# Kernel optimization log

Measured on AMD Instinct MI355X. Metric: run time of the kernel, lower is better.

## Reference

```python
import jax, jax.numpy as jnp
import numpy as np
from math import factorial, comb

N_NODES = 50000
N_EDGES = 640000
FEAT = 32
NUM_BASIS = 8
CUTOFF = 5.0
MAX_Z = 118
NUM_ITERS = 3
LMAX = 2
K = (LMAX + 1) ** 2  # 9 spherical channels for max_degree=2


def _assoc_legendre(c, s, lmax):
    # associated Legendre P_l^m without Condon-Shortley phase
    P = {(0, 0): np.ones_like(c)}
    for m in range(1, lmax + 1):
        P[(m, m)] = P[(m - 1, m - 1)] * (2 * m - 1) * s
    for m in range(lmax):
        P[(m + 1, m)] = (2 * m + 1) * c * P[(m, m)]
    for m in range(lmax + 1):
        for l in range(m + 2, lmax + 1):
            P[(l, m)] = ((2 * l - 1) * c * P[(l - 1, m)] - (l + m - 1) * P[(l - 2, m)]) / (l - m)
    return P


def _real_sh_np(xyz, lmax):
    # Racah-normalized real spherical harmonics (Y_00 = 1), order m=-l..l
    r = np.linalg.norm(xyz, axis=1)
    cth = xyz[:, 2] / r
    sth = np.sqrt(np.maximum(1.0 - cth ** 2, 0.0))
    phi = np.arctan2(xyz[:, 1], xyz[:, 0])
    P = _assoc_legendre(cth, sth, lmax)
    cols = []
    for l in range(lmax + 1):
        for m in range(-l, l + 1):
            am = abs(m)
            if m == 0:
                cols.append(P[(l, 0)])
            else:
                nrm = np.sqrt(2.0 * factorial(l - am) / factorial(l + am))
                ang = np.cos(am * phi) if m > 0 else np.sin(am * phi)
                cols.append(nrm * P[(l, am)] * ang)
    return np.stack(cols, axis=1)


def _gaunt_tensor():
    # cg[k1,k2,k3]: expansion of Y_k1 * Y_k2 onto Y_k3 (degrees <= 2).
    # Products of degree<=2 harmonics lie exactly in span of degree<=4 harmonics,
    # so the least-squares fit below recovers exact coefficients.
    rng = np.random.default_rng(0)
    pts = rng.normal(size=(4096, 3))
    pts /= np.linalg.norm(pts, axis=1, keepdims=True)
    A = _real_sh_np(pts, 2 * LMAX)  # (M, 25)
    Y = A[:, :K]                    # (M, 9)
    prod = (Y[:, :, None] * Y[:, None, :]).reshape(len(pts), K * K)
    coef, *_ = np.linalg.lstsq(A, prod, rcond=None)  # (25, 81)
    return coef[:K].reshape(K, K, K).transpose(1, 2, 0).astype(np.float32)


CG = jnp.asarray(_gaunt_tensor())  # (9, 9, 9)
LOG_BINOM = jnp.asarray([np.log(comb(NUM_BASIS - 1, kk)) for kk in range(NUM_BASIS)], dtype=jnp.float32)


def _sh_l2(u):
    # Racah real SH of unit vectors, degrees 0..2, order m=-l..l
    x, y, z = u[:, 0], u[:, 1], u[:, 2]
    s3 = 1.7320508075688772
    return jnp.stack([
        jnp.ones_like(x),
        y, z, x,
        s3 * x * y, s3 * y * z, 0.5 * (3.0 * z * z - 1.0), s3 * x * z, 0.5 * s3 * (x * x - y * y),
    ], axis=1)


def _radial(r):
    # reciprocal Bernstein basis (log-space, stable) * smooth cutoff
    u = r / (1.0 + r)
    k = jnp.arange(NUM_BASIS, dtype=jnp.float32)
    n = float(NUM_BASIS - 1)
    eps = 1e-12
    logu = jnp.log(jnp.maximum(u, eps))[:, None]
    log1u = jnp.log(jnp.maximum(1.0 - u, eps))[:, None]
    bern = jnp.exp(LOG_BINOM + k * logu + (n - k) * log1u)  # (E, B)
    cut = jnp.where(r < CUTOFF, jnp.exp(-(r * r) / jnp.maximum(CUTOFF * CUTOFF - r * r, eps)), 0.0)
    return bern * cut[:, None]


def _forward(dr_vec, embed, rad_w, d1w, d1b, d2w, d2b, Z, neighbor_idxs):
    idx_i, idx_j = neighbor_idxs[0], neighbor_idxs[1]
    r = jnp.linalg.norm(dr_vec, axis=1)
    u = dr_vec / jnp.maximum(r, 1e-9)[:, None]
    Ysh = _sh_l2(u)              # (E, 9) angular basis
    rad = _radial(r)             # (E, B) radial basis
    # mask padding edges (idx_i == idx_j) as in mask_by_neighbor
    rad = rad * (idx_i != idx_j).astype(rad.dtype)[:, None]

    N = Z.shape[0]
    x = jnp.zeros((N, K, FEAT), jnp.float32).at[:, 0, :].set(embed[Z])

    for i in range(NUM_ITERS):
        last = i == NUM_ITERS - 1
        k3 = 1 if last else K    # last MessagePass has max_degree=0
        xe = x[idx_j]                                  # (E, 9, F) edge gather
        g = jnp.einsum('eb,dbf->edf', rad, rad_w[i])   # (E, 3, F) radial->feature per basis degree
        y = jnp.zeros((N_EDGES, k3, FEAT), jnp.float32)
        for l2 in range(LMAX + 1):
            sl = slice(l2 * l2, (l2 + 1) ** 2)
            c = jnp.einsum('abc,eb->eac', CG[:, sl, :k3], Ysh[:, sl])          # (E, 9, k3)
            y = y + jnp.einsum('eac,eaf->ecf', c, xe * g[:, l2][:, None, :])   # (E, k3, F)
        m = jax.ops.segment_sum(y, idx_i, num_segments=N)                      # scatter-sum
        if last:
            x = x[:, :1, :]      # change_max_degree_or_type(x, 0)
        h = x + m
        h = jnp.einsum('nkf,fg->nkg', h, d1w[i]).at[:, 0, :].add(d1b[i])
        gate = jax.nn.sigmoid(h[:, :1, :])
        h = h * gate             # silu on scalar channel, sigmoid-gated tensor channels
        h = jnp.einsum('nkf,fg->nkg', h, d2w[i]).at[:, 0, :].add(d2b[i])
        x = x + h
    return x[:, 0, :]            # (N, F)


def setup_inputs() -> dict:
    key = jax.random.key(0)
    ks = jax.random.split(key, 8)
    dr_vec = jax.random.normal(ks[0], (N_EDGES, 3), jnp.float32) * 2.0
    Z = jax.random.randint(ks[1], (N_NODES,), 0, MAX_Z + 1, jnp.int32)
    neighbor_idxs = jax.random.randint(ks[2], (2, N_EDGES), 0, N_NODES, jnp.int32)
    embed = jax.random.normal(ks[3], (MAX_Z + 1, FEAT), jnp.float32)
    rad_w = jax.random.normal(ks[4], (NUM_ITERS, LMAX + 1, NUM_BASIS, FEAT), jnp.float32) * 0.5
    d1w = jax.random.normal(ks[5], (NUM_ITERS, FEAT, FEAT), jnp.float32) * (1.0 / np.sqrt(FEAT))
    d1b = jnp.zeros((NUM_ITERS, FEAT), jnp.float32)
    d2w = jax.random.normal(ks[6], (NUM_ITERS, FEAT, FEAT), jnp.float32) * 0.02
    d2b = jnp.zeros((NUM_ITERS, FEAT), jnp.float32)
    return {"dr_vec": dr_vec, "embed": embed, "rad_w": rad_w, "d1w": d1w, "d1b": d1b,
            "d2w": d2w, "d2b": d2b, "Z": Z, "neighbor_idxs": neighbor_idxs}


def reference(dr_vec, embed, rad_w, d1w, d1b, d2w, d2b, Z, neighbor_idxs):
    return _forward(dr_vec, embed, rad_w, d1w, d1b, d2w, d2b, Z, neighbor_idxs)
```

## Files before the change

kernel.cpp:

```cpp
#include <hip/hip_runtime.h>
#include <hip/hip_fp16.h>
#include <math.h>

#define NN 50000
#define NE 640000
#define F  32
#define KCH 9
#define CUT 5.0f

#define C13 (1.0f/3.0f)
#define C23 (2.0f/3.0f)
#define C15 0.2f
#define C25 0.4f
#define C17 (1.0f/7.0f)
#define C27 (2.0f/7.0f)
#define IS3 0.5773502691896258f
#define S35 0.3464101615137755f
#define S37 0.2474358296526968f
#define S3  1.7320508075688772f

#define XH_NODE_B 768

union U2H { unsigned int u; __half2 h; };

__device__ __forceinline__ unsigned int pack2(float a, float b) {
    U2H c; c.h = __floats2half2_rn(a, b); return c.u;
}
__device__ __forceinline__ float2 unpack2(unsigned int u) {
    U2H c; c.u = u; return __half22float2(c.h);
}

__global__ __launch_bounds__(256) void init_x(const float* __restrict__ embed,
                                              const int* __restrict__ Z,
                                              float* __restrict__ x,
                                              char* __restrict__ xh) {
    int idx = blockIdx.x * 256 + threadIdx.x;
    int n = idx >> 5, f = idx & 31;
    float v = embed[Z[n] * F + f];
    float* xp = x + (size_t)n * KCH * F + f;
    xp[0] = v;
    #pragma unroll
    for (int a = 1; a < KCH; ++a) xp[a * F] = 0.f;
    char* bp = xh + (size_t)n * XH_NODE_B + f * 24;
    uint2 u0; u0.x = pack2(v, 0.f); u0.y = 0u;
    uint2 zz; zz.x = 0u; zz.y = 0u;
    *(uint2*)bp = u0;
    *(uint2*)(bp + 8) = zz;
    *(uint2*)(bp + 16) = zz;
}

__global__ __launch_bounds__(256) void hist_kernel(const int* __restrict__ idx_i,
                                                   const int* __restrict__ idx_j,
                                                   const float* __restrict__ dr,
                                                   int* __restrict__ cnt) {
    int e = blockIdx.x * 256 + threadIdx.x;
    if (e >= NE) return;
    int ni = idx_i[e], nj = idx_j[e];
    float dx = dr[3 * e + 0], dy = dr[3 * e + 1], dz = dr[3 * e + 2];
    float r2 = fmaf(dx, dx, fmaf(dy, dy, dz * dz));
    if (ni != nj && r2 < CUT * CUT) atomicAdd(&cnt[ni], 1);
}

#define SCAN_T 1024
#define SCAN_C ((NN + SCAN_T - 1) / SCAN_T)

__global__ __launch_bounds__(SCAN_T) void scan_kernel(const int* __restrict__ cnt,
                                                      int* __restrict__ offs,
                                                      int* __restrict__ head) {
    __shared__ int ps[SCAN_T];
    int t = threadIdx.x;
    int b = t * SCAN_C;
    int e = min(b + SCAN_C, NN);
    int s = 0;
    for (int i = b; i < e; ++i) s += cnt[i];
    ps[t] = s;
    __syncthreads();
    for (int off = 1; off < SCAN_T; off <<= 1) {
        int v = (t >= off) ? ps[t - off] : 0;
        __syncthreads();
        ps[t] += v;
        __syncthreads();
    }
    int run = (t == 0) ? 0 : ps[t - 1];
    for (int i = b; i < e; ++i) { int c = cnt[i]; offs[i] = run; head[i] = run; run += c; }
    if (t == SCAN_T - 1) offs[NN] = ps[SCAN_T - 1];
}

__global__ __launch_bounds__(256) void fill_kernel(const int* __restrict__ idx_i,
                                                   const int* __restrict__ idx_j,
                                                   const float* __restrict__ dr,
                                                   int* __restrict__ head,
                                                   uint2* __restrict__ erec,
                                                   int* __restrict__ njarr) {
    int e = blockIdx.x * 256 + threadIdx.x;
    if (e >= NE) return;
    int ni = idx_i[e], nj = idx_j[e];
    float dx = dr[3 * e + 0], dy = dr[3 * e + 1], dz = dr[3 * e + 2];
    float r2 = fmaf(dx, dx, fmaf(dy, dy, dz * dz));
    if (!(ni != nj && r2 < CUT * CUT)) return;

    float r = sqrtf(r2);
    float inv = 1.0f / fmaxf(r, 1e-9f);
    float ux = dx * inv, uy = dy * inv, uz = dz * inv;

    float cut = expf(-r2 / fmaxf(CUT * CUT - r2, 1e-12f));
    float ur = r / (1.0f + r), vr = 1.0f - ur;
    float up2 = ur*ur, up3 = up2*ur, up4 = up3*ur, up5 = up4*ur, up6 = up5*ur, up7 = up6*ur;
    float vp2 = vr*vr, vp3 = vp2*vr, vp4 = vp3*vr, vp5 = vp4*vr, vp6 = vp5*vr, vp7 = vp6*vr;

    float rc0 = cut * vp7;
    float rc1 = cut * 7.f  * ur  * vp6;
    float rc2 = cut * 21.f * up2 * vp5;
    float rc3 = cut * 35.f * up3 * vp4;
    float rc4 = cut * 35.f * up4 * vp3;
    float rc5 = cut * 21.f * up5 * vp2;
    float rc6 = cut * 7.f  * up6 * vr;
    float rc7 = cut * up7;

    int p = atomicAdd(&head[ni], 1);
    uint2 e0, e1, e2;
    e0.x = pack2(ux, uy); e0.y = pack2(uz, 0.f);
    e1.x = pack2(rc0, rc1); e1.y = pack2(rc2, rc3);
    e2.x = pack2(rc4, rc5); e2.y = pack2(rc6, rc7);
    erec[(size_t)3 * p + 0] = e0;
    erec[(size_t)3 * p + 1] = e1;
    erec[(size_t)3 * p + 2] = e2;
    njarr[p] = nj;
}

template<int LAST>
__global__ __launch_bounds__(256) void gather_kernel(const uint2* __restrict__ erec,
                                                     const int* __restrict__ njarr,
                                                     const char* __restrict__ xh,
                                                     const float* __restrict__ rw_iter,
                                                     const int* __restrict__ offs,
                                                     float* __restrict__ m) {
    const int NWAVES = 2048 * 4;
    int lane = threadIdx.x & 63;
    int wid  = threadIdx.x >> 6;
    int half = lane >> 5;
    int f    = lane & 31;
    int gw   = blockIdx.x * 4 + wid;

    float rwv[24];
    #pragma unroll
    for (int lb = 0; lb < 24; ++lb) rwv[lb] = rw_iter[lb * F + f];
    if (LAST) {
        #pragma unroll
        for (int lb = 8; lb < 16; ++lb) rwv[lb] *= C13;
        #pragma unroll
        for (int lb = 16; lb < 24; ++lb) rwv[lb] *= C15;
    }

    constexpr int NACC = LAST ? 1 : KCH;

    for (int n = gw; n < NN; n += NWAVES) {
        int start = offs[n], end = offs[n + 1];

        float acc[NACC];
        #pragma unroll
        for (int a = 0; a < NACC; ++a) acc[a] = 0.f;

        int t = start + half;
        uint2 xa_c = {}, xb_c = {};
        unsigned int xc_c = 0;
        int nj_n = 0;

        if (t < end) {
            int nj0 = njarr[t];
            const char* bp = xh + (size_t)nj0 * XH_NODE_B + f * 24;
            xa_c = *(const uint2*)bp;
            xb_c = *(const uint2*)(bp + 8);
            xc_c = *(const unsigned int*)(bp + 16);
            int t2 = (t + 2 < end) ? t + 2 : t;
            nj_n = njarr[t2];
        }

        while (t < end) {
            int tn = t + 2;
            int tnc = (tn < end) ? tn : t;
            int tfc = (tn + 2 < end) ? tn + 2 : tnc;

            const char* bp = xh + (size_t)nj_n * XH_NODE_B + f * 24;
            uint2 xa_n = *(const uint2*)bp;
            uint2 xb_n = *(const uint2*)(bp + 8);
            unsigned int xc_n = *(const unsigned int*)(bp + 16);
            int nj_f = njarr[tfc];

            uint2 e0 = erec[(size_t)3 * t + 0];
            uint2 e1 = erec[(size_t)3 * t + 1];
            uint2 e2 = erec[(size_t)3 * t + 2];

            float2 uxy = unpack2(e0.x);
            float ux = uxy.x, uy = uxy.y;
            float uz = unpack2(e0.y).x;
            float2 rcA = unpack2(e1.x);
            float2 rcB = unpack2(e1.y);
            float2 rcC = unpack2(e2.x);
            float2 rcD = unpack2(e2.y);

            float xe[9];
            {
                float2 p;
                p = unpack2(xa_c.x); xe[0] = p.x; xe[1] = p.y;
                p = unpack2(xa_c.y); xe[2] = p.x; xe[3] = p.y;
                p = unpack2(xb_c.x); xe[4] = p.x; xe[5] = p.y;
                p = unpack2(xb_c.y); xe[6] = p.x; xe[7] = p.y;
                p = unpack2(xc_c);   xe[8] = p.x;
            }

            float g0, g1, g2;
            g0 = rcA.x * rwv[0];
            g0 = fmaf(rcA.y, rwv[1], g0); g0 = fmaf(rcB.x, rwv[2], g0); g0 = fmaf(rcB.y, rwv[3], g0);
            g0 = fmaf(rcC.x, rwv[4], g0); g0 = fmaf(rcC.y, rwv[5], g0); g0 = fmaf(rcD.x, rwv[6], g0);
            g0 = fmaf(rcD.y, rwv[7], g0);
            g1 = rcA.x * rwv[8];
            g1 = fmaf(rcA.y, rwv[9],  g1); g1 = fmaf(rcB.x, rwv[10], g1); g1 = fmaf(rcB.y, rwv[11], g1);
            g1 = fmaf(rcC.x, rwv[12], g1); g1 = fmaf(rcC.y, rwv[13], g1); g1 = fmaf(rcD.x, rwv[14], g1);
            g1 = fmaf(rcD.y, rwv[15], g1);
            g2 = rcA.x * rwv[16];
            g2 = fmaf(rcA.y, rwv[17], g2); g2 = fmaf(rcB.x, rwv[18], g2); g2 = fmaf(rcB.y, rwv[19], g2);
            g2 = fmaf(rcC.x, rwv[20], g2); g2 = fmaf(rcC.y, rwv[21], g2); g2 = fmaf(rcD.x, rwv[22], g2);
            g2 = fmaf(rcD.y, rwv[23], g2);

            if (LAST) {
                float dot1 = uy * xe[1];
                dot1 = fmaf(uz, xe[2], dot1);
                dot1 = fmaf(ux, xe[3], dot1);
                float Y4 = S3 * ux * uy, Y5 = S3 * uy * uz, Y7 = S3 * ux * uz;
                float Y6 = fmaf(1.5f * uz, uz, -0.5f);
                float Y8 = 0.5f * S3 * (ux * ux - uy * uy);
                float dot2 = Y4 * xe[4];
                dot2 = fmaf(Y5, xe[5], dot2);
                dot2 = fmaf(Y6, xe[6], dot2);
                dot2 = fmaf(Y7, xe[7], dot2);
                dot2 = fmaf(Y8, xe[8], dot2);
                acc[0] = fmaf(g0, xe[0], acc[0]);
                acc[0] = fmaf(g1, dot1, acc[0]);
                acc[0] = fmaf(g2, dot2, acc[0]);
            } else {
                float s2 = S3 * g2;
                float w[9];
                w[0] = g0;
                w[1] = uy * g1; w[2] = uz * g1; w[3] = ux * g1;
                w[4] = s2 * ux * uy;
                w[5] = s2 * uy * uz;
                w[6] = fmaf(1.5f * uz, uz, -0.5f) * g2;
                w[7] = s2 * ux * uz;
                w[8] = 0.5f * s2 * (ux * ux - uy * uy);

                float d0 = xe[0]*w[0], d1 = xe[1]*w[1], d2 = xe[2]*w[2], d3 = xe[3]*w[3];
                float d4 = xe[4]*w[4], d5 = xe[5]*w[5], d6 = xe[6]*w[6], d7 = xe[7]*w[7];
                float d8 = xe[8]*w[8];

                acc[0] += d0 + C13 * (d1 + d2 + d3) + C15 * (d4 + d5 + d6 + d7 + d8);
                #define T(a, b) (xe[a] * w[b] + xe[b] * w[a])
                acc[1] += T(0,1) - C15 * T(1,6) - S35 * T(1,8) + S35 * T(2,5) + S35 * T(3,4);
                acc[2] += T(0,2) + S35 * T(1,5) + C25 * T(2,6) + S35 * T(3,7);
                acc[3] += T(0,3) + S35 * T(1,4) + S35 * T(2,7) - C15 * T(3,6) + S35 * T(3,8);
                acc[4] += T(0,4) + IS3 * T(1,3) - C27 * T(4,6) + S37 * T(5,7);
                acc[5] += T(0,5) + IS3 * T(1,2) + S37 * T(4,7) + C17 * T(5,6) - S37 * T(5,8);
                acc[6] += T(0,6) - C13 * d1 + C23 * d2 - C13 * d3
                        - C27 * d4 + C17 * d5 + C27 * d6 + C17 * d7 - C27 * d8;
                acc[7] += T(0,7) + IS3 * T(2,3) + S37 * T(4,5) + C17 * T(6,7) + S37 * T(7,8);
                acc[8] += T(0,8) - IS3 * d1 + IS3 * d3 - S37 * d5 + S37 * d7 - C27 * T(6,8);
                #undef T
            }

            xa_c = xa_n; xb_c = xb_n; xc_c = xc_n;
            nj_n = nj_f;
            t = tn;
        }

        #pragma unroll
        for (int a = 0; a < NACC; ++a) acc[a] += __shfl_xor(acc[a], 32);

        if (half == 0) {
            if (LAST) {
                m[(size_t)n * F + f] = acc[0];
            } else {
                float* mp = m + (size_t)n * KCH * F + f;
                #pragma unroll
                for (int a = 0; a < KCH; ++a) mp[a * F] = acc[a];
            }
        }
    }
}

__global__ __launch_bounds__(256) void node_full(float* __restrict__ x,
                                                 const float* __restrict__ m,
                                                 char* __restrict__ xh,
                                                 const float* __restrict__ w1,
                                                 const float* __restrict__ b1,
                                                 const float* __restrict__ w2,
                                                 const float* __restrict__ b2) {
    __shared__ float tile[8][KCH][F];
    int nl = threadIdx.x >> 5, f = threadIdx.x & 31;
    int n = blockIdx.x * 8 + nl;

    float w1c[F];
    #pragma unroll
    for (int fi = 0; fi < F; ++fi) w1c[fi] = w1[fi * F + f];

    float xk[KCH];
    #pragma unroll
    for (int k = 0; k < KCH; ++k) {
        xk[k] = x[((size_t)n * KCH + k) * F + f];
        tile[nl][k][f] = xk[k] + m[((size_t)n * KCH + k) * F + f];
    }
    __syncthreads();

    float o1[KCH];
    #pragma unroll
    for (int k = 0; k < KCH; ++k) {
        float s = 0.f;
        #pragma unroll
        for (int fi = 0; fi < F; ++fi) s = fmaf(tile[nl][k][fi], w1c[fi], s);
        o1[k] = s;
    }
    o1[0] += b1[f];
    float gate = 1.0f / (1.0f + expf(-o1[0]));
    __syncthreads();
    #pragma unroll
    for (int k = 0; k < KCH; ++k) tile[nl][k][f] = o1[k] * gate;
    __syncthreads();

    float w2c[F];
    #pragma unroll
    for (int fi = 0; fi < F; ++fi) w2c[fi] = w2[fi * F + f];

    float xn[KCH];
    #pragma unroll
    for (int k = 0; k < KCH; ++k) {
        float s = (k == 0) ? b2[f] : 0.f;
        #pragma unroll
        for (int fi = 0; fi < F; ++fi) s = fmaf(tile[nl][k][fi], w2c[fi], s);
        xn[k] = xk[k] + s;
        x[((size_t)n * KCH + k) * F + f] = xn[k];
    }

    char* bp = xh + (size_t)n * XH_NODE_B + f * 24;
    uint2 u0, u1, u2;
    u0.x = pack2(xn[0], xn[1]); u0.y = pack2(xn[2], xn[3]);
    u1.x = pack2(xn[4], xn[5]); u1.y = pack2(xn[6], xn[7]);
    u2.x = pack2(xn[8], 0.f);   u2.y = 0u;
    *(uint2*)bp = u0;
    *(uint2*)(bp + 8) = u1;
    *(uint2*)(bp + 16) = u2;
}

__global__ __launch_bounds__(256) void node_last(const float* __restrict__ x,
                                                 const float* __restrict__ m1,
                                                 const float* __restrict__ w1,
                                                 const float* __restrict__ b1,
                                                 const float* __restrict__ w2,
                                                 const float* __restrict__ b2,
                                                 float* __restrict__ out) {
    __shared__ float tile[8][F];
    int nl = threadIdx.x >> 5, f = threadIdx.x & 31;
    int n = blockIdx.x * 8 + nl;

    float w1c[F];
    #pragma unroll
    for (int fi = 0; fi < F; ++fi) w1c[fi] = w1[fi * F + f];

    float x0 = x[(size_t)n * KCH * F + f];
    tile[nl][f] = x0 + m1[(size_t)n * F + f];
    __syncthreads();
    float s = 0.f;
    #pragma unroll
    for (int fi = 0; fi < F; ++fi) s = fmaf(tile[nl][fi], w1c[fi], s);
    s += b1[f];
    float gate = 1.0f / (1.0f + expf(-s));
    float h2 = s * gate;
    __syncthreads();
    tile[nl][f] = h2;
    __syncthreads();
    float w2c[F];
    #pragma unroll
    for (int fi = 0; fi < F; ++fi) w2c[fi] = w2[fi * F + f];
    float o = b2[f];
    #pragma unroll
    for (int fi = 0; fi < F; ++fi) o = fmaf(tile[nl][fi], w2c[fi], o);
    out[(size_t)n * F + f] = x0 + o;
}

extern "C" void kernel_launch(void* const* d_in, const int* in_sizes, int n_in,
                              void* d_out, int out_size, void* d_ws, size_t ws_size,
                              hipStream_t stream) {
    (void)in_sizes; (void)n_in; (void)out_size; (void)ws_size;
    const float* dr    = (const float*)d_in[0];
    const float* embed = (const float*)d_in[1];
    const float* rad_w = (const float*)d_in[2];
    const float* d1w   = (const float*)d_in[3];
    const float* d1b   = (const float*)d_in[4];
    const float* d2w   = (const float*)d_in[5];
    const float* d2b   = (const float*)d_in[6];
    const int*   Z     = (const int*)d_in[7];
    const int*   nidx  = (const int*)d_in[8];
    const int* idx_i = nidx;
    const int* idx_j = nidx + NE;

    float* x = (float*)d_ws;
    float* m = x + (size_t)NN * KCH * F;
    char*  xh = (char*)(m + (size_t)NN * KCH * F);
    uint2* erec = (uint2*)(xh + (size_t)NN * XH_NODE_B);
    int* njarr = (int*)(erec + (size_t)3 * NE);
    int* offs = njarr + NE;
    int* head = offs + (NN + 1);
    int* cnt  = head + NN;
    float* outp = (float*)d_out;

    hipMemsetAsync(cnt, 0, NN * sizeof(int), stream);
    hist_kernel<<<(NE + 255) / 256, 256, 0, stream>>>(idx_i, idx_j, dr, cnt);
    scan_kernel<<<1, SCAN_T, 0, stream>>>(cnt, offs, head);
    fill_kernel<<<(NE + 255) / 256, 256, 0, stream>>>(idx_i, idx_j, dr, head, erec, njarr);

    init_x<<<NN * F / 256, 256, 0, stream>>>(embed, Z, x, xh);

    for (int i = 0; i < 3; ++i) {
        const float* rwi = rad_w + (size_t)i * 3 * 8 * F;
        const float* w1 = d1w + (size_t)i * F * F;
        const float* b1 = d1b + (size_t)i * F;
        const float* w2 = d2w + (size_t)i * F * F;
        const float* b2 = d2b + (size_t)i * F;
        if (i < 2) {
            gather_kernel<0><<<2048, 256, 0, stream>>>(erec, njarr, xh, rwi, offs, m);
            node_full<<<NN / 8, 256, 0, stream>>>(x, m, xh, w1, b1, w2, b2);
        } else {
            gather_kernel<1><<<2048, 256, 0, stream>>>(erec, njarr, xh, rwi, offs, m);
            node_last<<<NN / 8, 256, 0, stream>>>(x, m, w1, b1, w2, b2, outp);
        }
    }
}
```

Baseline: 694.5 us.

## Pack neighbor index into edge record, split fp16 node layout, specialize first gather

The neighbor index is now stored in the upper 16 bits of the first edge-record word, which removes the separate njarr array and its loads. The half-precision node features move from a padded 24-byte-per-feature layout to a 16-byte uint4 array plus a separate 2-byte array, so each gather fetch is an aligned vector load and uses less memory traffic. The first iteration gets its own gather mode: only channel 0 is nonzero after initialization, so it reads a single fp16 scalar per neighbor and skips the full Gaunt product. Storing the index in 16 bits only works while the node count stays below 65536.

Result: faster. 583.5 us (-16.0%).

```diff
diff --git a/kernel.cpp b/kernel.cpp
--- a/kernel.cpp
+++ b/kernel.cpp
@@ -19,8 +19,6 @@
 #define S37 0.2474358296526968f
 #define S3  1.7320508075688772f
 
-#define XH_NODE_B 768
-
 union U2H { unsigned int u; __half2 h; };
 
 __device__ __forceinline__ unsigned int pack2(float a, float b) {
@@ -33,7 +31,7 @@
 __global__ __launch_bounds__(256) void init_x(const float* __restrict__ embed,
                                               const int* __restrict__ Z,
                                               float* __restrict__ x,
-                                              char* __restrict__ xh) {
+                                              __half* __restrict__ x0h) {
     int idx = blockIdx.x * 256 + threadIdx.x;
     int n = idx >> 5, f = idx & 31;
     float v = embed[Z[n] * F + f];
@@ -41,12 +39,7 @@
     xp[0] = v;
     #pragma unroll
     for (int a = 1; a < KCH; ++a) xp[a * F] = 0.f;
-    char* bp = xh + (size_t)n * XH_NODE_B + f * 24;
-    uint2 u0; u0.x = pack2(v, 0.f); u0.y = 0u;
-    uint2 zz; zz.x = 0u; zz.y = 0u;
-    *(uint2*)bp = u0;
-    *(uint2*)(bp + 8) = zz;
-    *(uint2*)(bp + 16) = zz;
+    x0h[idx] = __float2half_rn(v);
 }
 
 __global__ __launch_bounds__(256) void hist_kernel(const int* __restrict__ idx_i,
@@ -90,8 +83,7 @@
                                                    const int* __restrict__ idx_j,
                                                    const float* __restrict__ dr,
                                                    int* __restrict__ head,
-                                                   uint2* __restrict__ erec,
-                                                   int* __restrict__ njarr) {
+                                                   uint2* __restrict__ erec) {
     int e = blockIdx.x * 256 + threadIdx.x;
     if (e >= NE) return;
     int ni = idx_i[e], nj = idx_j[e];
@@ -119,19 +111,21 @@
 
     int p = atomicAdd(&head[ni], 1);
     uint2 e0, e1, e2;
-    e0.x = pack2(ux, uy); e0.y = pack2(uz, 0.f);
+    U2H zh; zh.h = __floats2half2_rn(uz, 0.f);
+    e0.x = pack2(ux, uy);
+    e0.y = (zh.u & 0xFFFFu) | ((unsigned int)nj << 16);
     e1.x = pack2(rc0, rc1); e1.y = pack2(rc2, rc3);
     e2.x = pack2(rc4, rc5); e2.y = pack2(rc6, rc7);
     erec[(size_t)3 * p + 0] = e0;
     erec[(size_t)3 * p + 1] = e1;
     erec[(size_t)3 * p + 2] = e2;
-    njarr[p] = nj;
-}
-
-template<int LAST>
+}
+
+template<int MODE>
 __global__ __launch_bounds__(256) void gather_kernel(const uint2* __restrict__ erec,
-                                                     const int* __restrict__ njarr,
-                                                     const char* __restrict__ xh,
+                                                     const __half* __restrict__ x0h,
+                                                     const uint4* __restrict__ xhA,
+                                                     const ushort* __restrict__ xhB,
                                                      const float* __restrict__ rw_iter,
                                                      const int* __restrict__ offs,
                                                      float* __restrict__ m) {
@@ -145,14 +139,14 @@
     float rwv[24];
     #pragma unroll
     for (int lb = 0; lb < 24; ++lb) rwv[lb] = rw_iter[lb * F + f];
-    if (LAST) {
+    if (MODE == 2) {
         #pragma unroll
         for (int lb = 8; lb < 16; ++lb) rwv[lb] *= C13;
         #pragma unroll
         for (int lb = 16; lb < 24; ++lb) rwv[lb] *= C15;
     }
 
-    constexpr int NACC = LAST ? 1 : KCH;
+    constexpr int NACC = (MODE == 2) ? 1 : KCH;
 
     for (int n = gw; n < NN; n += NWAVES) {
         int start = offs[n], end = offs[n + 1];
@@ -162,18 +156,21 @@
         for (int a = 0; a < NACC; ++a) acc[a] = 0.f;
 
         int t = start + half;
-        uint2 xa_c = {}, xb_c = {};
-        unsigned int xc_c = 0;
-        int nj_n = 0;
+        uint2 e0_c = {}, e0_n = {};
+        uint4 xa_c = {};
+        ushort x8_c = 0;
 
         if (t < end) {
-            int nj0 = njarr[t];
-            const char* bp = xh + (size_t)nj0 * XH_NODE_B + f * 24;
-            xa_c = *(const uint2*)bp;
-            xb_c = *(const uint2*)(bp + 8);
-            xc_c = *(const unsigned int*)(bp + 16);
+            e0_c = erec[(size_t)3 * t + 0];
+            int nj0 = (int)(e0_c.y >> 16);
+            if (MODE == 0) {
+                x8_c = __half_as_ushort(x0h[nj0 * F + f]);
+            } else {
+                xa_c = xhA[nj0 * F + f];
+                x8_c = xhB[nj0 * F + f];
+            }
             int t2 = (t + 2 < end) ? t + 2 : t;
-            nj_n = njarr[t2];
+            e0_n = erec[(size_t)3 * t2 + 0];
         }
 
         while (t < end) {
@@ -181,33 +178,27 @@
             int tnc = (tn < end) ? tn : t;
             int tfc = (tn + 2 < end) ? tn + 2 : tnc;
 
-            const char* bp = xh + (size_t)nj_n * XH_NODE_B + f * 24;
-            uint2 xa_n = *(const uint2*)bp;
-            uint2 xb_n = *(const uint2*)(bp + 8);
-            unsigned int xc_n = *(const unsigned int*)(bp + 16);
-            int nj_f = njarr[tfc];
-
-            uint2 e0 = erec[(size_t)3 * t + 0];
+            int njn = (int)(e0_n.y >> 16);
+            uint4 xa_n = {};
+            ushort x8_n;
+            if (MODE == 0) {
+                x8_n = __half_as_ushort(x0h[njn * F + f]);
+            } else {
+                xa_n = xhA[njn * F + f];
+                x8_n = xhB[njn * F + f];
+            }
+            uint2 e0_f = erec[(size_t)3 * tfc + 0];
+
             uint2 e1 = erec[(size_t)3 * t + 1];
             uint2 e2 = erec[(size_t)3 * t + 2];
 
-            float2 uxy = unpack2(e0.x);
+            float2 uxy = unpack2(e0_c.x);
             float ux = uxy.x, uy = uxy.y;
-            float uz = unpack2(e0.y).x;
+            float uz = unpack2(e0_c.y).x;
             float2 rcA = unpack2(e1.x);
             float2 rcB = unpack2(e1.y);
             float2 rcC = unpack2(e2.x);
             float2 rcD = unpack2(e2.y);
-
-            float xe[9];
-            {
-                float2 p;
-                p = unpack2(xa_c.x); xe[0] = p.x; xe[1] = p.y;
-                p = unpack2(xa_c.y); xe[2] = p.x; xe[3] = p.y;
-                p = unpack2(xb_c.x); xe[4] = p.x; xe[5] = p.y;
-                p = unpack2(xb_c.y); xe[6] = p.x; xe[7] = p.y;
-                p = unpack2(xc_c);   xe[8] = p.x;
-            }
 
             float g0, g1, g2;
             g0 = rcA.x * rwv[0];
@@ -223,52 +214,75 @@
             g2 = fmaf(rcC.x, rwv[20], g2); g2 = fmaf(rcC.y, rwv[21], g2); g2 = fmaf(rcD.x, rwv[22], g2);
             g2 = fmaf(rcD.y, rwv[23], g2);
 
-            if (LAST) {
-                float dot1 = uy * xe[1];
-                dot1 = fmaf(uz, xe[2], dot1);
-                dot1 = fmaf(ux, xe[3], dot1);
-                float Y4 = S3 * ux * uy, Y5 = S3 * uy * uz, Y7 = S3 * ux * uz;
-                float Y6 = fmaf(1.5f * uz, uz, -0.5f);
-                float Y8 = 0.5f * S3 * (ux * ux - uy * uy);
-                float dot2 = Y4 * xe[4];
-                dot2 = fmaf(Y5, xe[5], dot2);
-                dot2 = fmaf(Y6, xe[6], dot2);
-                dot2 = fmaf(Y7, xe[7], dot2);
-                dot2 = fmaf(Y8, xe[8], dot2);
-                acc[0] = fmaf(g0, xe[0], acc[0]);
-                acc[0] = fmaf(g1, dot1, acc[0]);
-                acc[0] = fmaf(g2, dot2, acc[0]);
+            if (MODE == 0) {
+                float xe0 = __half2float(__ushort_as_half(x8_c));
+                float s2 = S3 * g2;
+                acc[0] = fmaf(xe0, g0, acc[0]);
+                acc[1] = fmaf(xe0, uy * g1, acc[1]);
+                acc[2] = fmaf(xe0, uz * g1, acc[2]);
+                acc[3] = fmaf(xe0, ux * g1, acc[3]);
+                acc[4] = fmaf(xe0, s2 * ux * uy, acc[4]);
+                acc[5] = fmaf(xe0, s2 * uy * uz, acc[5]);
+                acc[6] = fmaf(xe0, fmaf(1.5f * uz, uz, -0.5f) * g2, acc[6]);
+                acc[7] = fmaf(xe0, s2 * ux * uz, acc[7]);
+                acc[8] = fmaf(xe0, 0.5f * s2 * (ux * ux - uy * uy), acc[8]);
             } else {
-                float s2 = S3 * g2;
-                float w[9];
-                w[0] = g0;
-                w[1] = uy * g1; w[2] = uz * g1; w[3] = ux * g1;
-                w[4] = s2 * ux * uy;
-                w[5] = s2 * uy * uz;
-                w[6] = fmaf(1.5f * uz, uz, -0.5f) * g2;
-                w[7] = s2 * ux * uz;
-                w[8] = 0.5f * s2 * (ux * ux - uy * uy);
-
-                float d0 = xe[0]*w[0], d1 = xe[1]*w[1], d2 = xe[2]*w[2], d3 = xe[3]*w[3];
-                float d4 = xe[4]*w[4], d5 = xe[5]*w[5], d6 = xe[6]*w[6], d7 = xe[7]*w[7];
-                float d8 = xe[8]*w[8];
-
-                acc[0] += d0 + C13 * (d1 + d2 + d3) + C15 * (d4 + d5 + d6 + d7 + d8);
-                #define T(a, b) (xe[a] * w[b] + xe[b] * w[a])
-                acc[1] += T(0,1) - C15 * T(1,6) - S35 * T(1,8) + S35 * T(2,5) + S35 * T(3,4);
-                acc[2] += T(0,2) + S35 * T(1,5) + C25 * T(2,6) + S35 * T(3,7);
-                acc[3] += T(0,3) + S35 * T(1,4) + S35 * T(2,7) - C15 * T(3,6) + S35 * T(3,8);
-                acc[4] += T(0,4) + IS3 * T(1,3) - C27 * T(4,6) + S37 * T(5,7);
-                acc[5] += T(0,5) + IS3 * T(1,2) + S37 * T(4,7) + C17 * T(5,6) - S37 * T(5,8);
-                acc[6] += T(0,6) - C13 * d1 + C23 * d2 - C13 * d3
-                        - C27 * d4 + C17 * d5 + C27 * d6 + C17 * d7 - C27 * d8;
-                acc[7] += T(0,7) + IS3 * T(2,3) + S37 * T(4,5) + C17 * T(6,7) + S37 * T(7,8);
-                acc[8] += T(0,8) - IS3 * d1 + IS3 * d3 - S37 * d5 + S37 * d7 - C27 * T(6,8);
-                #undef T
+                float xe[9];
+                {
+                    float2 p;
+                    p = unpack2(xa_c.x); xe[0] = p.x; xe[1] = p.y;
+                    p = unpack2(xa_c.y); xe[2] = p.x; xe[3] = p.y;
+                    p = unpack2(xa_c.z); xe[4] = p.x; xe[5] = p.y;
+                    p = unpack2(xa_c.w); xe[6] = p.x; xe[7] = p.y;
+                    xe[8] = __half2float(__ushort_as_half(x8_c));
+                }
+                if (MODE == 2) {
+                    float dot1 = uy * xe[1];
+                    dot1 = fmaf(uz, xe[2], dot1);
+                    dot1 = fmaf(ux, xe[3], dot1);
+                    float Y4 = S3 * ux * uy, Y5 = S3 * uy * uz, Y7 = S3 * ux * uz;
+                    float Y6 = fmaf(1.5f * uz, uz, -0.5f);
+                    float Y8 = 0.5f * S3 * (ux * ux - uy * uy);
+                    float dot2 = Y4 * xe[4];
+                    dot2 = fmaf(Y5, xe[5], dot2);
+                    dot2 = fmaf(Y6, xe[6], dot2);
+                    dot2 = fmaf(Y7, xe[7], dot2);
+                    dot2 = fmaf(Y8, xe[8], dot2);
+                    acc[0] = fmaf(g0, xe[0], acc[0]);
+                    acc[0] = fmaf(g1, dot1, acc[0]);
+                    acc[0] = fmaf(g2, dot2, acc[0]);
+                } else {
+                    float s2 = S3 * g2;
+                    float w[9];
+                    w[0] = g0;
+                    w[1] = uy * g1; w[2] = uz * g1; w[3] = ux * g1;
+                    w[4] = s2 * ux * uy;
+                    w[5] = s2 * uy * uz;
+                    w[6] = fmaf(1.5f * uz, uz, -0.5f) * g2;
+                    w[7] = s2 * ux * uz;
+                    w[8] = 0.5f * s2 * (ux * ux - uy * uy);
+
+                    float d0 = xe[0]*w[0], d1 = xe[1]*w[1], d2 = xe[2]*w[2], d3 = xe[3]*w[3];
+                    float d4 = xe[4]*w[4], d5 = xe[5]*w[5], d6 = xe[6]*w[6], d7 = xe[7]*w[7];
+                    float d8 = xe[8]*w[8];
+
+                    acc[0] += d0 + C13 * (d1 + d2 + d3) + C15 * (d4 + d5 + d6 + d7 + d8);
+                    #define T(a, b) (xe[a] * w[b] + xe[b] * w[a])
+                    acc[1] += T(0,1) - C15 * T(1,6) - S35 * T(1,8) + S35 * T(2,5) + S35 * T(3,4);
+                    acc[2] += T(0,2) + S35 * T(1,5) + C25 * T(2,6) + S35 * T(3,7);
+                    acc[3] += T(0,3) + S35 * T(1,4) + S35 * T(2,7) - C15 * T(3,6) + S35 * T(3,8);
+                    acc[4] += T(0,4) + IS3 * T(1,3) - C27 * T(4,6) + S37 * T(5,7);
+                    acc[5] += T(0,5) + IS3 * T(1,2) + S37 * T(4,7) + C17 * T(5,6) - S37 * T(5,8);
+                    acc[6] += T(0,6) - C13 * d1 + C23 * d2 - C13 * d3
+                            - C27 * d4 + C17 * d5 + C27 * d6 + C17 * d7 - C27 * d8;
+                    acc[7] += T(0,7) + IS3 * T(2,3) + S37 * T(4,5) + C17 * T(6,7) + S37 * T(7,8);
+                    acc[8] += T(0,8) - IS3 * d1 + IS3 * d3 - S37 * d5 + S37 * d7 - C27 * T(6,8);
+                    #undef T
+                }
             }
 
-            xa_c = xa_n; xb_c = xb_n; xc_c = xc_n;
-            nj_n = nj_f;
+            e0_c = e0_n; e0_n = e0_f;
+            xa_c = xa_n; x8_c = x8_n;
             t = tn;
         }
 
@@ -276,7 +290,7 @@
         for (int a = 0; a < NACC; ++a) acc[a] += __shfl_xor(acc[a], 32);
 
         if (half == 0) {
-            if (LAST) {
+            if (MODE == 2) {
                 m[(size_t)n * F + f] = acc[0];
             } else {
                 float* mp = m + (size_t)n * KCH * F + f;
@@ -289,7 +303,8 @@
 
 __global__ __launch_bounds__(256) void node_full(float* __restrict__ x,
                                                  const float* __restrict__ m,
-                                                 char* __restrict__ xh,
+                                                 uint4* __restrict__ xhA,
+                                                 ushort* __restrict__ xhB,
                                                  const float* __restrict__ w1,
                                                  const float* __restrict__ b1,
                                                  const float* __restrict__ w2,
@@ -339,14 +354,11 @@
         x[((size_t)n * KCH + k) * F + f] = xn[k];
     }
 
-    char* bp = xh + (size_t)n * XH_NODE_B + f * 24;
-    uint2 u0, u1, u2;
-    u0.x = pack2(xn[0], xn[1]); u0.y = pack2(xn[2], xn[3]);
-    u1.x = pack2(xn[4], xn[5]); u1.y = pack2(xn[6], xn[7]);
-    u2.x = pack2(xn[8], 0.f);   u2.y = 0u;
-    *(uint2*)bp = u0;
-    *(uint2*)(bp + 8) = u1;
-    *(uint2*)(bp + 16) = u2;
+    uint4 ua;
+    ua.x = pack2(xn[0], xn[1]); ua.y = pack2(xn[2], xn[3]);
+    ua.z = pack2(xn[4], xn[5]); ua.w = pack2(xn[6], xn[7]);
+    xhA[n * F + f] = ua;
+    xhB[n * F + f] = __half_as_ushort(__float2half_rn(xn[8]));
 }
 
 __global__ __launch_bounds__(256) void node_last(const float* __restrict__ x,
@@ -401,12 +413,13 @@
     const int* idx_i = nidx;
     const int* idx_j = nidx + NE;
 
-    float* x = (float*)d_ws;
-    float* m = x + (size_t)NN * KCH * F;
-    char*  xh = (char*)(m + (size_t)NN * KCH * F);
-    uint2* erec = (uint2*)(xh + (size_t)NN * XH_NODE_B);
-    int* njarr = (int*)(erec + (size_t)3 * NE);
-    int* offs = njarr + NE;
+    float* x   = (float*)d_ws;
+    float* m   = x + (size_t)NN * KCH * F;
+    uint4* xhA = (uint4*)(m + (size_t)NN * KCH * F);
+    __half* x0h = (__half*)(xhA + (size_t)NN * F);
+    ushort* xhB = (ushort*)(x0h + (size_t)NN * F);
+    uint2* erec = (uint2*)(xhB + (size_t)NN * F);
+    int* offs = (int*)(erec + (size_t)3 * NE);
     int* head = offs + (NN + 1);
     int* cnt  = head + NN;
     float* outp = (float*)d_out;
@@ -414,9 +427,9 @@
     hipMemsetAsync(cnt, 0, NN * sizeof(int), stream);
     hist_kernel<<<(NE + 255) / 256, 256, 0, stream>>>(idx_i, idx_j, dr, cnt);
     scan_kernel<<<1, SCAN_T, 0, stream>>>(cnt, offs, head);
-    fill_kernel<<<(NE + 255) / 256, 256, 0, stream>>>(idx_i, idx_j, dr, head, erec, njarr);
-
-    init_x<<<NN * F / 256, 256, 0, stream>>>(embed, Z, x, xh);
+    fill_kernel<<<(NE + 255) / 256, 256, 0, stream>>>(idx_i, idx_j, dr, head, erec);
+
+    init_x<<<NN * F / 256, 256, 0, stream>>>(embed, Z, x, x0h);
 
     for (int i = 0; i < 3; ++i) {
         const float* rwi = rad_w + (size_t)i * 3 * 8 * F;
@@ -424,11 +437,14 @@
         const float* b1 = d1b + (size_t)i * F;
         const float* w2 = d2w + (size_t)i * F * F;
         const float* b2 = d2b + (size_t)i * F;
-        if (i < 2) {
-            gather_kernel<0><<<2048, 256, 0, stream>>>(erec, njarr, xh, rwi, offs, m);
-            node_full<<<NN / 8, 256, 0, stream>>>(x, m, xh, w1, b1, w2, b2);
+        if (i == 0) {
+            gather_kernel<0><<<2048, 256, 0, stream>>>(erec, x0h, xhA, xhB, rwi, offs, m);
+            node_full<<<NN / 8, 256, 0, stream>>>(x, m, xhA, xhB, w1, b1, w2, b2);
+        } else if (i == 1) {
+            gather_kernel<1><<<2048, 256, 0, stream>>>(erec, x0h, xhA, xhB, rwi, offs, m);
+            node_full<<<NN / 8, 256, 0, stream>>>(x, m, xhA, xhB, w1, b1, w2, b2);
         } else {
-            gather_kernel<1><<<2048, 256, 0, stream>>>(erec, njarr, xh, rwi, offs, m);
+            gather_kernel<2><<<2048, 256, 0, stream>>>(erec, x0h, xhA, xhB, rwi, offs, m);
             node_last<<<NN / 8, 256, 0, stream>>>(x, m, w1, b1, w2, b2, outp);
         }
     }
```
